# Kernel tuning notes

Hardware: AMD Instinct MI355X
Metric: run time of the kernel (lower is better)

## Reference

```python
import jax, jax.numpy as jnp
import numpy as np

NEG = -1.0e9


def setup_inputs() -> dict:
    key = jax.random.key(0)
    ks = jax.random.split(key, 8)
    B, L, D = 4, 2048, 1024
    s = 1.0 / np.sqrt(D)
    return {
        "x": jax.random.normal(ks[0], (B, L, D), dtype=jnp.float32),
        "Wq": jax.random.normal(ks[1], (D, D), dtype=jnp.float32) * s,
        "bq": jax.random.normal(ks[2], (D,), dtype=jnp.float32) * 0.02,
        "Wk": jax.random.normal(ks[3], (D, D), dtype=jnp.float32) * s,
        "bk": jax.random.normal(ks[4], (D,), dtype=jnp.float32) * 0.02,
        "Wv": jax.random.normal(ks[5], (D, D), dtype=jnp.float32) * s,
        "bv": jax.random.normal(ks[6], (D,), dtype=jnp.float32) * 0.02,
        "lengths": jax.random.randint(ks[7], (B,), 1, 2048, dtype=jnp.int32),
    }


def reference(x, Wq, bq, Wk, bk, Wv, bv, lengths):
    # x: [B, L, D]; single-head self-attention with causal + length additive masks
    B, L, D = x.shape
    q = x @ Wq + bq  # [B, L, D]
    k = x @ Wk + bk
    v = x @ Wv + bv
    scale = 1.0 / jnp.sqrt(jnp.asarray(D, dtype=x.dtype))
    att = jnp.einsum("bid,bjd->bij", q, k) * scale  # [B, L, L]
    idx = jnp.arange(L)
    causal = jnp.where(idx[None, :] > idx[:, None], NEG, 0.0).astype(x.dtype)  # [L, L]
    # length mask: NEG where j >= len[b] or i >= len[b]
    invalid = (idx[None, :] >= lengths[:, None])  # [B, L]
    lenmask = jnp.where(invalid[:, :, None] | invalid[:, None, :], NEG, 0.0).astype(x.dtype)
    att = att + causal[None, :, :] + lenmask
    att = jax.nn.softmax(att, axis=-1)
    return jnp.einsum("bij,bjd->bid", att, v)
```

## Files before the change

### kernel.cpp

```cpp
#include <hip/hip_runtime.h>

#define NEGV (-1.0e9f)

typedef __bf16 bf16_t;
typedef __bf16 bf16x8 __attribute__((ext_vector_type(8)));
typedef __bf16 bf16x4 __attribute__((ext_vector_type(4)));
typedef float  f32x4  __attribute__((ext_vector_type(4)));

__device__ __forceinline__ void gld16(const void* g, void* l) {
    __builtin_amdgcn_global_load_lds(
        (const __attribute__((address_space(1))) void*)g,
        (__attribute__((address_space(3))) void*)l, 16, 0, 0);
}


#define STG(P0, P1, BASE, NB, HOFS) do {               \
    gld16(P0, (BASE) + (NB) * 32768 + (HOFS));         \
    gld16(P1, (BASE) + (NB) * 32768 + (HOFS) + 8192);  \
    P0 += 64; P1 += 64; } while (0)

#define MMROW(ai)                                                                                    \
    acc[ib + ai][0] = __builtin_amdgcn_mfma_f32_16x16x32_bf16(a##ai, b0, acc[ib + ai][0], 0, 0, 0);  \
    acc[ib + ai][1] = __builtin_amdgcn_mfma_f32_16x16x32_bf16(a##ai, b1, acc[ib + ai][1], 0, 0, 0);  \
    acc[ib + ai][2] = __builtin_amdgcn_mfma_f32_16x16x32_bf16(a##ai, b2, acc[ib + ai][2], 0, 0, 0);  \
    acc[ib + ai][3] = __builtin_amdgcn_mfma_f32_16x16x32_bf16(a##ai, b3, acc[ib + ai][3], 0, 0, 0)

#define PHASE(BUFO, HOFS, PK, STAGE_STMT, ENDW) do {                     \
    bf16x8 a0 = *(const bf16x8*)(rdA + (BUFO) + (HOFS)        + (PK));   \
    bf16x8 a1 = *(const bf16x8*)(rdA + (BUFO) + (HOFS) + 2048 + (PK));   \
    bf16x8 a2 = *(const bf16x8*)(rdA + (BUFO) + (HOFS) + 4096 + (PK));   \
    bf16x8 a3 = *(const bf16x8*)(rdA + (BUFO) + (HOFS) + 6144 + (PK));   \
    bf16x8 b0 = *(const bf16x8*)(rdB + (BUFO)          + (PK));          \
    bf16x8 b1 = *(const bf16x8*)(rdB + (BUFO) + 2048   + (PK));          \
    bf16x8 b2 = *(const bf16x8*)(rdB + (BUFO) + 4096   + (PK));          \
    bf16x8 b3 = *(const bf16x8*)(rdB + (BUFO) + 6144   + (PK));          \
    STAGE_STMT;                                                          \
    __builtin_amdgcn_s_barrier();                                        \
    asm volatile("s_waitcnt lgkmcnt(0)" ::: "memory");                   \
    __builtin_amdgcn_s_setprio(1);                                       \
    {                                                                    \
        const int ib = (HOFS) ? 4 : 0;                                   \
        MMROW(0); MMROW(1); MMROW(2); MMROW(3);                          \
    }                                                                    \
    __builtin_amdgcn_s_setprio(0);                                       \
    ENDW;                                                                \
    __builtin_amdgcn_s_barrier();                                        \
} while (0)

__device__ __forceinline__ void mainloop256(
    const bf16_t* __restrict__ A, const bf16_t* __restrict__ B,
    int ldA, int ldB, int nkt, char* smem, int tid, f32x4 acc[8][4])
{
    const int w    = tid >> 6;
    const int lane = tid & 63;
    const int wm   = w & 1;
    const int wn   = w >> 1;
    const int l16  = lane & 15;
    const int quad = lane >> 4;

    const int r0 = tid >> 3;
    const int c0 = ((tid & 7) ^ (r0 & 7)) * 8;
    const int s1 = 512 + tid;
    const int r1 = s1 >> 3;
    const int c1 = ((s1 & 7) ^ (r1 & 7)) * 8;

    const bf16_t* pa00 = A + (size_t)(r0)       * ldA + c0;
    const bf16_t* pa01 = A + (size_t)(r1)       * ldA + c1;
    const bf16_t* pa10 = A + (size_t)(128 + r0) * ldA + c0;
    const bf16_t* pa11 = A + (size_t)(128 + r1) * ldA + c1;
    const bf16_t* pb00 = B + (size_t)(r0)       * ldB + c0;
    const bf16_t* pb01 = B + (size_t)(r1)       * ldB + c1;
    const bf16_t* pb10 = B + (size_t)(128 + r0) * ldB + c0;
    const bf16_t* pb11 = B + (size_t)(128 + r1) * ldB + c1;

    char* const stA = smem + (w << 10);
    char* const stB = smem + 65536 + (w << 10);

    const int pk0 = ((quad    ) ^ (l16 & 7)) << 4;
    const int pk1 = ((quad + 4) ^ (l16 & 7)) << 4;
    const char* rdA = smem +         ((wm << 7) + l16) * 128;
    const char* rdB = smem + 65536 + ((wn << 6) + l16) * 128;

    STG(pa00, pa01, stA, 0, 0);
    STG(pa10, pa11, stA, 0, 16384);
    STG(pb00, pb01, stB, 0, 0);
    STG(pb10, pb11, stB, 0, 16384);
    asm volatile("s_waitcnt vmcnt(0)" ::: "memory");
    __builtin_amdgcn_s_barrier();

    for (int kt = 0; kt < nkt; ++kt) {
        const int bufo = (kt & 1) << 15;
        const int nb   = (kt & 1) ^ 1;
        const bool st  = (kt + 1) < nkt;
        PHASE(bufo, 0,    pk0, if (st) STG(pa00, pa01, stA, nb, 0),     );
        PHASE(bufo, 0,    pk1, if (st) STG(pa10, pa11, stA, nb, 16384), );
        PHASE(bufo, 8192, pk0, if (st) STG(pb00, pb01, stB, nb, 0),     );
        PHASE(bufo, 8192, pk1, if (st) STG(pb10, pb11, stB, nb, 16384),
              asm volatile("s_waitcnt vmcnt(0)" ::: "memory"));
    }
}

__global__ __launch_bounds__(256)
void convert_x_kernel(const float* __restrict__ x, bf16_t* __restrict__ xb)
{
    const size_t i = ((size_t)blockIdx.x * 256 + threadIdx.x) * 8;
    float4 a = *(const float4*)&x[i];
    float4 b = *(const float4*)&x[i + 4];
    bf16x8 o;
    o[0] = (bf16_t)a.x; o[1] = (bf16_t)a.y; o[2] = (bf16_t)a.z; o[3] = (bf16_t)a.w;
    o[4] = (bf16_t)b.x; o[5] = (bf16_t)b.y; o[6] = (bf16_t)b.z; o[7] = (bf16_t)b.w;
    *(bf16x8*)&xb[i] = o;
}

__global__ __launch_bounds__(256)
void transpose_w_kernel(const float* __restrict__ W0, const float* __restrict__ W1,
                        const float* __restrict__ W2, bf16_t* __restrict__ WT)
{
    __shared__ float t[32][33];
    const float* W = (blockIdx.z == 0) ? W0 : (blockIdx.z == 1) ? W1 : W2;
    bf16_t* WTz = WT + (size_t)blockIdx.z * 1024 * 1024;
    const int k0 = blockIdx.y * 32, n0 = blockIdx.x * 32;
    const int r = threadIdx.x >> 3, c4 = (threadIdx.x & 7) * 4;
    float4 v = *(const float4*)&W[(size_t)(k0 + r) * 1024 + n0 + c4];
    t[r][c4 + 0] = v.x; t[r][c4 + 1] = v.y; t[r][c4 + 2] = v.z; t[r][c4 + 3] = v.w;
    __syncthreads();
    bf16x4 o;
#pragma unroll
    for (int j = 0; j < 4; ++j) o[j] = (bf16_t)t[c4 + j][r];
    *(bf16x4*)&WTz[(size_t)(n0 + r) * 1024 + k0 + c4] = o;
}

__global__ __launch_bounds__(512, 2)
void gemm_qk256(const bf16_t* __restrict__ A, const bf16_t* __restrict__ Bt,
                const float* __restrict__ bq, const float* __restrict__ bk,
                bf16_t* __restrict__ C, int N, int Kd)
{
    __shared__ __align__(16) char smem[131072];
    int bid = blockIdx.y * 8 + blockIdx.x;
    bid = (bid & 7) * 32 + (bid >> 3);
    const int n0 = (bid & 7) * 256;
    const int m0 = (bid >> 3) * 256;
    const int tid = threadIdx.x;

    f32x4 acc[8][4];
#pragma unroll
    for (int i = 0; i < 8; ++i)
#pragma unroll
        for (int j = 0; j < 4; ++j) acc[i][j] = (f32x4)(0.0f);

    mainloop256(A + (size_t)m0 * Kd, Bt + (size_t)n0 * Kd, Kd, Kd, Kd >> 6,
                smem, tid, acc);

    const int w = tid >> 6, lane = tid & 63;
    const int wm = w & 1, wn = w >> 1, quad = lane >> 4, l16 = lane & 15;
#pragma unroll
    for (int j = 0; j < 4; ++j) {
        const int col = n0 + wn * 64 + j * 16 + l16;
        const float bval = (col < 1024) ? bq[col] : bk[col - 1024];
#pragma unroll
        for (int i = 0; i < 8; ++i) {
            const int row = m0 + wm * 128 + i * 16 + quad * 4;
#pragma unroll
            for (int r = 0; r < 4; ++r)
                C[(size_t)(row + r) * N + col] = (bf16_t)(acc[i][j][r] + bval);
        }
    }
}

__global__ __launch_bounds__(512, 2)
void gemm_vt256(const bf16_t* __restrict__ WvT, const bf16_t* __restrict__ xb,
                const float* __restrict__ bv, bf16_t* __restrict__ VT,
                int N, int Kd)
{
    __shared__ __align__(16) char smem[131072];
    const int m0 = blockIdx.y * 256, n0 = blockIdx.x * 256;
    const int tid = threadIdx.x;

    f32x4 acc[8][4];
#pragma unroll
    for (int i = 0; i < 8; ++i)
#pragma unroll
        for (int j = 0; j < 4; ++j) acc[i][j] = (f32x4)(0.0f);

    mainloop256(WvT + (size_t)m0 * Kd, xb + (size_t)n0 * Kd, Kd, Kd, Kd >> 6,
                smem, tid, acc);

    const int w = tid >> 6, lane = tid & 63;
    const int wm = w & 1, wn = w >> 1, quad = lane >> 4, l16 = lane & 15;
#pragma unroll
    for (int i = 0; i < 8; ++i) {
        const int row = m0 + wm * 128 + i * 16 + quad * 4;
#pragma unroll
        for (int r = 0; r < 4; ++r) {
            const float bval = bv[row + r];
#pragma unroll
            for (int j = 0; j < 4; ++j) {
                const int col = n0 + wn * 64 + j * 16 + l16;
                VT[(size_t)(row + r) * N + col] = (bf16_t)(acc[i][j][r] + bval);
            }
        }
    }
}

__global__ __launch_bounds__(512, 2)
void scores256(const bf16_t* __restrict__ Q, const bf16_t* __restrict__ K,
               int ldq, const int* __restrict__ lengths,
               float* __restrict__ S, int L, int Dd, float alpha)
{
    __shared__ __align__(16) char smem[131072];
    const int b = blockIdx.z;
    const int len = lengths[b];
    int it = 0;
    while ((it + 1) * (it + 2) / 2 <= (int)blockIdx.x) ++it;
    const int jt = blockIdx.x - it * (it + 1) / 2;
    const int m0 = it * 256, n0 = jt * 256;
    float* Sb = S + (size_t)b * L * L;
    const int tid = threadIdx.x;

    f32x4 acc[8][4];
#pragma unroll
    for (int i = 0; i < 8; ++i)
#pragma unroll
        for (int j = 0; j < 4; ++j) acc[i][j] = (f32x4)(0.0f);

    const bf16_t* Qb = Q + (size_t)b * L * ldq + (size_t)m0 * ldq;
    const bf16_t* Kb = K + (size_t)b * L * ldq + (size_t)n0 * ldq;
    mainloop256(Qb, Kb, ldq, ldq, Dd >> 6, smem, tid, acc);

    const int w = tid >> 6, lane = tid & 63;
    const int wm = w & 1, wn = w >> 1, quad = lane >> 4, l16 = lane & 15;
#pragma unroll
    for (int i = 0; i < 8; ++i) {
#pragma unroll
        for (int j = 0; j < 4; ++j) {
            const int col = n0 + wn * 64 + j * 16 + l16;
#pragma unroll
            for (int r = 0; r < 4; ++r) {
                const int row = m0 + wm * 128 + i * 16 + quad * 4 + r;
                float s = acc[i][j][r] * alpha;
                if (col > row) s += NEGV;
                if (row >= len || col >= len) s += NEGV;
                Sb[(size_t)row * L + col] = s;
            }
        }
    }
}

__global__ __launch_bounds__(256)
void softmax_kernel(const float* __restrict__ S, bf16_t* __restrict__ P,
                    int L, int ldp)
{
    __shared__ float red[8];
    const int i = blockIdx.x;
    const int bound  = ((i >> 7) + 1) << 7;
    const int bound2 = ((i >> 8) + 1) << 8;
    const float* row = S + ((size_t)blockIdx.y * L + i) * L;
    bf16_t* prow = P + ((size_t)blockIdx.y * L + i) * ldp;
    const int t = threadIdx.x;
    const int w = t >> 6, lane = t & 63;
    const int j8 = t * 8;
    const bool act = j8 < bound;

    float v[8];
    float m = -3.0e38f;
    if (act) {
        float4 a = *(const float4*)&row[j8];
        float4 b = *(const float4*)&row[j8 + 4];
        v[0] = a.x; v[1] = a.y; v[2] = a.z; v[3] = a.w;
        v[4] = b.x; v[5] = b.y; v[6] = b.z; v[7] = b.w;
#pragma unroll
        for (int j = 0; j < 8; ++j) m = fmaxf(m, v[j]);
    }
#pragma unroll
    for (int off = 32; off > 0; off >>= 1) m = fmaxf(m, __shfl_down(m, off, 64));
    if (lane == 0) red[w] = m;
    __syncthreads();
    m = fmaxf(fmaxf(red[0], red[1]), fmaxf(red[2], red[3]));

    float s = 0.f;
    if (act) {
#pragma unroll
        for (int j = 0; j < 8; ++j) {
            v[j] = __expf(v[j] - m);
            s += v[j];
        }
    }
#pragma unroll
    for (int off = 32; off > 0; off >>= 1) s += __shfl_down(s, off, 64);
    if (lane == 0) red[4 + w] = s;
    __syncthreads();
    s = red[4] + red[5] + red[6] + red[7];

    if (act) {
        const float inv = 1.0f / s;
        bf16x8 o;
#pragma unroll
        for (int j = 0; j < 8; ++j) o[j] = (bf16_t)(v[j] * inv);
        *(bf16x8*)&prow[j8] = o;
    } else if (j8 < bound2) {
        bf16x8 z;
#pragma unroll
        for (int j = 0; j < 8; ++j) z[j] = (bf16_t)0.0f;
        *(bf16x8*)&prow[j8] = z;
    }
}

__global__ __launch_bounds__(512, 2)
void pv256(const bf16_t* __restrict__ P, int ldp,
           const bf16_t* __restrict__ VT, int ldv,
           float* __restrict__ O, int L, int Dd)
{
    __shared__ __align__(16) char smem[131072];
    const int b = blockIdx.z;
    const int mt = gridDim.y - 1 - blockIdx.y;
    const int m0 = mt * 256, n0 = blockIdx.x * 256;
    const int tid = threadIdx.x;

    f32x4 acc[8][4];
#pragma unroll
    for (int i = 0; i < 8; ++i)
#pragma unroll
        for (int j = 0; j < 4; ++j) acc[i][j] = (f32x4)(0.0f);

    const int nkt = (m0 + 256) >> 6;
    const bf16_t* Pb = P + (size_t)b * L * ldp + (size_t)m0 * ldp;
    const bf16_t* Vb = VT + (size_t)b * L + (size_t)n0 * ldv;
    mainloop256(Pb, Vb, ldp, ldv, nkt, smem, tid, acc);

    float* Ob = O + (size_t)b * L * Dd;
    const int w = tid >> 6, lane = tid & 63;
    const int wm = w & 1, wn = w >> 1, quad = lane >> 4, l16 = lane & 15;
#pragma unroll
    for (int i = 0; i < 8; ++i) {
        const int row = m0 + wm * 128 + i * 16 + quad * 4;
#pragma unroll
        for (int j = 0; j < 4; ++j) {
            const int col = n0 + wn * 64 + j * 16 + l16;
#pragma unroll
            for (int r = 0; r < 4; ++r)
                Ob[(size_t)(row + r) * Dd + col] = acc[i][j][r];
        }
    }
}

extern "C" void kernel_launch(void* const* d_in, const int* in_sizes, int n_in,
                              void* d_out, int out_size, void* d_ws, size_t ws_size,
                              hipStream_t stream)
{
    const float* x  = (const float*)d_in[0];
    const float* Wq = (const float*)d_in[1];
    const float* bq = (const float*)d_in[2];
    const float* Wk = (const float*)d_in[3];
    const float* bk = (const float*)d_in[4];
    const float* Wv = (const float*)d_in[5];
    const float* bv = (const float*)d_in[6];
    const int*  len = (const int*)d_in[7];
    float* out = (float*)d_out;

    const int B = 4, L = 2048, D = 1024;
    const int M = B * L;
    const int N2 = 2 * D;

    bf16_t* xb = (bf16_t*)d_ws;
    bf16_t* WT = xb + (size_t)M * D;
    bf16_t* QK = WT + (size_t)3 * D * D;
    bf16_t* VT = QK + (size_t)M * N2;
    float*  S  = (float*)(VT + (size_t)D * M);
    bf16_t* P  = QK;

    convert_x_kernel<<<(M * D) / 2048, 256, 0, stream>>>(x, xb);

    transpose_w_kernel<<<dim3(32, 32, 3), 256, 0, stream>>>(Wq, Wk, Wv, WT);

    gemm_qk256<<<dim3(8, 32), 512, 0, stream>>>(xb, WT, bq, bk, QK, N2, D);

    gemm_vt256<<<dim3(32, 4), 512, 0, stream>>>(
        WT + (size_t)2 * D * D, xb, bv, VT, M, D);

    scores256<<<dim3(36, 1, B), 512, 0, stream>>>(
        QK, QK + 1024, N2, len, S, L, D, 0.03125f);

    softmax_kernel<<<dim3(L, B), 256, 0, stream>>>(S, P, L, N2);

    pv256<<<dim3(4, 8, 4), 512, 0, stream>>>(P, N2, VT, M, out, L, D);
}
```

Measured before the change: 280.7 us.

## Use 256x128 GEMM tiles for V projection, scores and PV kernels

Adds a new 256x128 tiled mainloop with its own LDS staging and MFMA phase structure, and switches the V projection, causal scores and PV GEMMs to it with doubled grid sizes. The intent is to fill more of the GPU's compute units, since the earlier 256x256 grids (128, 144 and 128 blocks) underfilled the device. Smaller tiles lower arithmetic intensity and raise global and LDS traffic per FLOP. The scores kernel's triangular block indexing is rewritten for two column tiles per row tile.

```diff
diff --git a/kernel.cpp b/kernel.cpp
--- a/kernel.cpp
+++ b/kernel.cpp
@@ -100,6 +100,88 @@
     }
 }
 
+
+#define STG2(P0, P1, DST) do {                                   \
+    gld16(P0, (DST)); gld16(P1, (char*)(DST) + 8192);            \
+    P0 += 64; P1 += 64; } while (0)
+
+#define MM2ROW(ai)                                                                         \
+    acc[ai][0] = __builtin_amdgcn_mfma_f32_16x16x32_bf16(a##ai, b0, acc[ai][0], 0, 0, 0);  \
+    acc[ai][1] = __builtin_amdgcn_mfma_f32_16x16x32_bf16(a##ai, b1, acc[ai][1], 0, 0, 0);  \
+    acc[ai][2] = __builtin_amdgcn_mfma_f32_16x16x32_bf16(a##ai, b2, acc[ai][2], 0, 0, 0);  \
+    acc[ai][3] = __builtin_amdgcn_mfma_f32_16x16x32_bf16(a##ai, b3, acc[ai][3], 0, 0, 0)
+
+#define PHASEX(AOFS, BOFS, PK, STAGE_STMT, ENDW) do {                  \
+    bf16x8 a0 = *(const bf16x8*)(rdA + (AOFS)        + (PK));          \
+    bf16x8 a1 = *(const bf16x8*)(rdA + (AOFS) + 2048 + (PK));          \
+    bf16x8 a2 = *(const bf16x8*)(rdA + (AOFS) + 4096 + (PK));          \
+    bf16x8 a3 = *(const bf16x8*)(rdA + (AOFS) + 6144 + (PK));          \
+    bf16x8 b0 = *(const bf16x8*)(rdB + (BOFS)        + (PK));          \
+    bf16x8 b1 = *(const bf16x8*)(rdB + (BOFS) + 2048 + (PK));          \
+    bf16x8 b2 = *(const bf16x8*)(rdB + (BOFS) + 4096 + (PK));          \
+    bf16x8 b3 = *(const bf16x8*)(rdB + (BOFS) + 6144 + (PK));          \
+    STAGE_STMT;                                                        \
+    __builtin_amdgcn_s_barrier();                                      \
+    asm volatile("s_waitcnt lgkmcnt(0)" ::: "memory");                 \
+    __builtin_amdgcn_s_setprio(1);                                     \
+    MM2ROW(0); MM2ROW(1); MM2ROW(2); MM2ROW(3);                        \
+    __builtin_amdgcn_s_setprio(0);                                     \
+    ENDW;                                                              \
+    __builtin_amdgcn_s_barrier();                                      \
+} while (0)
+
+__device__ __forceinline__ void mainloop256x128(
+    const bf16_t* __restrict__ A, const bf16_t* __restrict__ B,
+    int ldA, int ldB, int nkt, char* smem, int tid, f32x4 acc[4][4])
+{
+    const int w    = tid >> 6;
+    const int lane = tid & 63;
+    const int wm   = w & 3;
+    const int wn   = w >> 2;
+    const int l16  = lane & 15;
+    const int quad = lane >> 4;
+
+    const int r0 = tid >> 3;
+    const int c0 = ((tid & 7) ^ (r0 & 7)) * 8;
+    const int s1 = 512 + tid;
+    const int r1 = s1 >> 3;
+    const int c1 = ((s1 & 7) ^ (r1 & 7)) * 8;
+
+    const bf16_t* pa00 = A + (size_t)(r0)       * ldA + c0;
+    const bf16_t* pa01 = A + (size_t)(r1)       * ldA + c1;
+    const bf16_t* pa10 = A + (size_t)(128 + r0) * ldA + c0;
+    const bf16_t* pa11 = A + (size_t)(128 + r1) * ldA + c1;
+    const bf16_t* pb0  = B + (size_t)(r0)       * ldB + c0;
+    const bf16_t* pb1  = B + (size_t)(r1)       * ldB + c1;
+
+    char* const stA = smem + (w << 10);
+    char* const stB = smem + 65536 + (w << 10);
+
+    const int pk0 = ((quad    ) ^ (l16 & 7)) << 4;
+    const int pk1 = ((quad + 4) ^ (l16 & 7)) << 4;
+    const char* rdA = smem +         ((wm << 6) + l16) * 128;
+    const char* rdB = smem + 65536 + ((wn << 6) + l16) * 128;
+
+    STG2(pa00, pa01, stA);
+    STG2(pa10, pa11, stA + 16384);
+    STG2(pb0,  pb1,  stB);
+    asm volatile("s_waitcnt vmcnt(0)" ::: "memory");
+    __builtin_amdgcn_s_barrier();
+
+    for (int kt = 0; kt < nkt; ++kt) {
+        const int aofs = (kt & 1) << 15;
+        const int bofs = (kt & 1) << 14;
+        char* const nA = stA + ((((kt & 1) ^ 1)) << 15);
+        char* const nB = stB + ((((kt & 1) ^ 1)) << 14);
+        const bool st  = (kt + 1) < nkt;
+        PHASEX(aofs, bofs, pk0,
+               if (st) { STG2(pa00, pa01, nA); STG2(pa10, pa11, nA + 16384); }, );
+        PHASEX(aofs, bofs, pk1,
+               if (st) { STG2(pb0, pb1, nB); },
+               asm volatile("s_waitcnt vmcnt(0)" ::: "memory"));
+    }
+}
+
 __global__ __launch_bounds__(256)
 void convert_x_kernel(const float* __restrict__ x, bf16_t* __restrict__ xb)
 {
@@ -172,24 +254,25 @@
                 const float* __restrict__ bv, bf16_t* __restrict__ VT,
                 int N, int Kd)
 {
-    __shared__ __align__(16) char smem[131072];
-    const int m0 = blockIdx.y * 256, n0 = blockIdx.x * 256;
+    __shared__ __align__(16) char smem[98304];
+    const int m0 = blockIdx.y * 256;
+    const int n0 = blockIdx.x * 128;
     const int tid = threadIdx.x;
 
-    f32x4 acc[8][4];
-#pragma unroll
-    for (int i = 0; i < 8; ++i)
+    f32x4 acc[4][4];
+#pragma unroll
+    for (int i = 0; i < 4; ++i)
 #pragma unroll
         for (int j = 0; j < 4; ++j) acc[i][j] = (f32x4)(0.0f);
 
-    mainloop256(WvT + (size_t)m0 * Kd, xb + (size_t)n0 * Kd, Kd, Kd, Kd >> 6,
-                smem, tid, acc);
+    mainloop256x128(WvT + (size_t)m0 * Kd, xb + (size_t)n0 * Kd, Kd, Kd, Kd >> 6,
+                    smem, tid, acc);
 
     const int w = tid >> 6, lane = tid & 63;
-    const int wm = w & 1, wn = w >> 1, quad = lane >> 4, l16 = lane & 15;
-#pragma unroll
-    for (int i = 0; i < 8; ++i) {
-        const int row = m0 + wm * 128 + i * 16 + quad * 4;
+    const int wm = w & 3, wn = w >> 2, quad = lane >> 4, l16 = lane & 15;
+#pragma unroll
+    for (int i = 0; i < 4; ++i) {
+        const int row = m0 + wm * 64 + i * 16 + quad * 4;
 #pragma unroll
         for (int r = 0; r < 4; ++r) {
             const float bval = bv[row + r];
@@ -207,36 +290,36 @@
                int ldq, const int* __restrict__ lengths,
                float* __restrict__ S, int L, int Dd, float alpha)
 {
-    __shared__ __align__(16) char smem[131072];
+    __shared__ __align__(16) char smem[98304];
     const int b = blockIdx.z;
     const int len = lengths[b];
-    int it = 0;
-    while ((it + 1) * (it + 2) / 2 <= (int)blockIdx.x) ++it;
-    const int jt = blockIdx.x - it * (it + 1) / 2;
-    const int m0 = it * 256, n0 = jt * 256;
+    int mt = 0;
+    while ((mt + 1) * (mt + 2) <= (int)blockIdx.x) ++mt;
+    const int jt = blockIdx.x - mt * (mt + 1);
+    const int m0 = mt * 256, n0 = jt * 128;
     float* Sb = S + (size_t)b * L * L;
     const int tid = threadIdx.x;
 
-    f32x4 acc[8][4];
-#pragma unroll
-    for (int i = 0; i < 8; ++i)
+    f32x4 acc[4][4];
+#pragma unroll
+    for (int i = 0; i < 4; ++i)
 #pragma unroll
         for (int j = 0; j < 4; ++j) acc[i][j] = (f32x4)(0.0f);
 
     const bf16_t* Qb = Q + (size_t)b * L * ldq + (size_t)m0 * ldq;
     const bf16_t* Kb = K + (size_t)b * L * ldq + (size_t)n0 * ldq;
-    mainloop256(Qb, Kb, ldq, ldq, Dd >> 6, smem, tid, acc);
+    mainloop256x128(Qb, Kb, ldq, ldq, Dd >> 6, smem, tid, acc);
 
     const int w = tid >> 6, lane = tid & 63;
-    const int wm = w & 1, wn = w >> 1, quad = lane >> 4, l16 = lane & 15;
-#pragma unroll
-    for (int i = 0; i < 8; ++i) {
+    const int wm = w & 3, wn = w >> 2, quad = lane >> 4, l16 = lane & 15;
+#pragma unroll
+    for (int i = 0; i < 4; ++i) {
 #pragma unroll
         for (int j = 0; j < 4; ++j) {
             const int col = n0 + wn * 64 + j * 16 + l16;
 #pragma unroll
             for (int r = 0; r < 4; ++r) {
-                const int row = m0 + wm * 128 + i * 16 + quad * 4 + r;
+                const int row = m0 + wm * 64 + i * 16 + quad * 4 + r;
                 float s = acc[i][j][r] * alpha;
                 if (col > row) s += NEGV;
                 if (row >= len || col >= len) s += NEGV;
@@ -310,29 +393,29 @@
            const bf16_t* __restrict__ VT, int ldv,
            float* __restrict__ O, int L, int Dd)
 {
-    __shared__ __align__(16) char smem[131072];
+    __shared__ __align__(16) char smem[98304];
     const int b = blockIdx.z;
     const int mt = gridDim.y - 1 - blockIdx.y;
-    const int m0 = mt * 256, n0 = blockIdx.x * 256;
+    const int m0 = mt * 256, n0 = blockIdx.x * 128;
     const int tid = threadIdx.x;
 
-    f32x4 acc[8][4];
-#pragma unroll
-    for (int i = 0; i < 8; ++i)
+    f32x4 acc[4][4];
+#pragma unroll
+    for (int i = 0; i < 4; ++i)
 #pragma unroll
         for (int j = 0; j < 4; ++j) acc[i][j] = (f32x4)(0.0f);
 
     const int nkt = (m0 + 256) >> 6;
     const bf16_t* Pb = P + (size_t)b * L * ldp + (size_t)m0 * ldp;
     const bf16_t* Vb = VT + (size_t)b * L + (size_t)n0 * ldv;
-    mainloop256(Pb, Vb, ldp, ldv, nkt, smem, tid, acc);
+    mainloop256x128(Pb, Vb, ldp, ldv, nkt, smem, tid, acc);
 
     float* Ob = O + (size_t)b * L * Dd;
     const int w = tid >> 6, lane = tid & 63;
-    const int wm = w & 1, wn = w >> 1, quad = lane >> 4, l16 = lane & 15;
-#pragma unroll
-    for (int i = 0; i < 8; ++i) {
-        const int row = m0 + wm * 128 + i * 16 + quad * 4;
+    const int wm = w & 3, wn = w >> 2, quad = lane >> 4, l16 = lane & 15;
+#pragma unroll
+    for (int i = 0; i < 4; ++i) {
+        const int row = m0 + wm * 64 + i * 16 + quad * 4;
 #pragma unroll
         for (int j = 0; j < 4; ++j) {
             const int col = n0 + wn * 64 + j * 16 + l16;
@@ -374,13 +457,13 @@
 
     gemm_qk256<<<dim3(8, 32), 512, 0, stream>>>(xb, WT, bq, bk, QK, N2, D);
 
-    gemm_vt256<<<dim3(32, 4), 512, 0, stream>>>(
+    gemm_vt256<<<dim3(64, 4), 512, 0, stream>>>(
         WT + (size_t)2 * D * D, xb, bv, VT, M, D);
 
-    scores256<<<dim3(36, 1, B), 512, 0, stream>>>(
+    scores256<<<dim3(72, 1, B), 512, 0, stream>>>(
         QK, QK + 1024, N2, len, S, L, D, 0.03125f);
 
     softmax_kernel<<<dim3(L, B), 256, 0, stream>>>(S, P, L, N2);
 
-    pv256<<<dim3(4, 8, 4), 512, 0, stream>>>(P, N2, VT, M, out, L, D);
-}
+    pv256<<<dim3(8, 8, 4), 512, 0, stream>>>(P, N2, VT, M, out, L, D);
+}
```

After: 259.9 us. -7.4%, faster.

## Rework GEMM mainloop to triple-buffered BK=32 and 256x128 tiles for V/PV

Applied to the files above, without the earlier changes.

Replaces the shared double-buffered 64-wide-K mainloop with a triple-buffered 32-wide-K pipeline that prefetches two stages ahead and needs one barrier per iteration instead of several. It splits LDS fragment waits so the first half of the MFMAs can start before all reads land. It also adds a 256x128 tile variant for the V projection and PV kernels, which doubles their grids and adds block-index swizzling. The goal is to hide global-to-LDS latency, cut barrier stalls and improve load balance, at the cost of more loop iterations and a new LDS swizzle layout that must stay conflict-free.

```diff
diff --git a/kernel.cpp b/kernel.cpp
--- a/kernel.cpp
+++ b/kernel.cpp
@@ -14,90 +14,142 @@
 }
 
 
-#define STG(P0, P1, BASE, NB, HOFS) do {               \
-    gld16(P0, (BASE) + (NB) * 32768 + (HOFS));         \
-    gld16(P1, (BASE) + (NB) * 32768 + (HOFS) + 8192);  \
-    P0 += 64; P1 += 64; } while (0)
-
-#define MMROW(ai)                                                                                    \
-    acc[ib + ai][0] = __builtin_amdgcn_mfma_f32_16x16x32_bf16(a##ai, b0, acc[ib + ai][0], 0, 0, 0);  \
-    acc[ib + ai][1] = __builtin_amdgcn_mfma_f32_16x16x32_bf16(a##ai, b1, acc[ib + ai][1], 0, 0, 0);  \
-    acc[ib + ai][2] = __builtin_amdgcn_mfma_f32_16x16x32_bf16(a##ai, b2, acc[ib + ai][2], 0, 0, 0);  \
-    acc[ib + ai][3] = __builtin_amdgcn_mfma_f32_16x16x32_bf16(a##ai, b3, acc[ib + ai][3], 0, 0, 0)
-
-#define PHASE(BUFO, HOFS, PK, STAGE_STMT, ENDW) do {                     \
-    bf16x8 a0 = *(const bf16x8*)(rdA + (BUFO) + (HOFS)        + (PK));   \
-    bf16x8 a1 = *(const bf16x8*)(rdA + (BUFO) + (HOFS) + 2048 + (PK));   \
-    bf16x8 a2 = *(const bf16x8*)(rdA + (BUFO) + (HOFS) + 4096 + (PK));   \
-    bf16x8 a3 = *(const bf16x8*)(rdA + (BUFO) + (HOFS) + 6144 + (PK));   \
-    bf16x8 b0 = *(const bf16x8*)(rdB + (BUFO)          + (PK));          \
-    bf16x8 b1 = *(const bf16x8*)(rdB + (BUFO) + 2048   + (PK));          \
-    bf16x8 b2 = *(const bf16x8*)(rdB + (BUFO) + 4096   + (PK));          \
-    bf16x8 b3 = *(const bf16x8*)(rdB + (BUFO) + 6144   + (PK));          \
-    STAGE_STMT;                                                          \
-    __builtin_amdgcn_s_barrier();                                        \
-    asm volatile("s_waitcnt lgkmcnt(0)" ::: "memory");                   \
-    __builtin_amdgcn_s_setprio(1);                                       \
-    {                                                                    \
-        const int ib = (HOFS) ? 4 : 0;                                   \
-        MMROW(0); MMROW(1); MMROW(2); MMROW(3);                          \
-    }                                                                    \
-    __builtin_amdgcn_s_setprio(0);                                       \
-    ENDW;                                                                \
-    __builtin_amdgcn_s_barrier();                                        \
-} while (0)
-
-__device__ __forceinline__ void mainloop256(
+#define MMR(AF, IB)                                                                        \
+    acc[IB][0] = __builtin_amdgcn_mfma_f32_16x16x32_bf16(AF, b0, acc[IB][0], 0, 0, 0);     \
+    acc[IB][1] = __builtin_amdgcn_mfma_f32_16x16x32_bf16(AF, b1, acc[IB][1], 0, 0, 0);     \
+    acc[IB][2] = __builtin_amdgcn_mfma_f32_16x16x32_bf16(AF, b2, acc[IB][2], 0, 0, 0);     \
+    acc[IB][3] = __builtin_amdgcn_mfma_f32_16x16x32_bf16(AF, b3, acc[IB][3], 0, 0, 0)
+
+__device__ __forceinline__ void ml256x256(
     const bf16_t* __restrict__ A, const bf16_t* __restrict__ B,
     int ldA, int ldB, int nkt, char* smem, int tid, f32x4 acc[8][4])
 {
-    const int w    = tid >> 6;
-    const int lane = tid & 63;
-    const int wm   = w & 1;
-    const int wn   = w >> 1;
-    const int l16  = lane & 15;
-    const int quad = lane >> 4;
-
-    const int r0 = tid >> 3;
-    const int c0 = ((tid & 7) ^ (r0 & 7)) * 8;
-    const int s1 = 512 + tid;
-    const int r1 = s1 >> 3;
-    const int c1 = ((s1 & 7) ^ (r1 & 7)) * 8;
-
-    const bf16_t* pa00 = A + (size_t)(r0)       * ldA + c0;
-    const bf16_t* pa01 = A + (size_t)(r1)       * ldA + c1;
-    const bf16_t* pa10 = A + (size_t)(128 + r0) * ldA + c0;
-    const bf16_t* pa11 = A + (size_t)(128 + r1) * ldA + c1;
-    const bf16_t* pb00 = B + (size_t)(r0)       * ldB + c0;
-    const bf16_t* pb01 = B + (size_t)(r1)       * ldB + c1;
-    const bf16_t* pb10 = B + (size_t)(128 + r0) * ldB + c0;
-    const bf16_t* pb11 = B + (size_t)(128 + r1) * ldB + c1;
-
+    const int w = tid >> 6, lane = tid & 63;
+    const int wm = w & 1, wn = w >> 1;
+    const int l16 = lane & 15, quad = lane >> 4;
+
+    const int g0 = 2 * (tid >> 3) + ((tid >> 2) & 1);
+    const int c0 = ((tid & 3) ^ ((tid >> 3) & 3)) * 8;
+    const bf16_t* pa0 = A + (size_t)g0 * ldA + c0;
+    const bf16_t* pa1 = pa0 + (size_t)128 * ldA;
+    const bf16_t* pb0 = B + (size_t)g0 * ldB + c0;
+    const bf16_t* pb1 = pb0 + (size_t)128 * ldB;
     char* const stA = smem + (w << 10);
-    char* const stB = smem + 65536 + (w << 10);
-
-    const int pk0 = ((quad    ) ^ (l16 & 7)) << 4;
-    const int pk1 = ((quad + 4) ^ (l16 & 7)) << 4;
-    const char* rdA = smem +         ((wm << 7) + l16) * 128;
-    const char* rdB = smem + 65536 + ((wn << 6) + l16) * 128;
-
-    STG(pa00, pa01, stA, 0, 0);
-    STG(pa10, pa11, stA, 0, 16384);
-    STG(pb00, pb01, stB, 0, 0);
-    STG(pb10, pb11, stB, 0, 16384);
-    asm volatile("s_waitcnt vmcnt(0)" ::: "memory");
+    char* const stB = smem + 16384 + (w << 10);
+
+    const int rowo = (l16 >> 1) * 128 + (l16 & 1) * 64 + ((quad ^ ((l16 >> 1) & 3)) << 4);
+    const char* rdA = smem + (wm << 13) + rowo;
+    const char* rdB = smem + 16384 + (wn << 12) + rowo;
+
+#define STG6(BO) do { gld16(pa0, stA + (BO)); gld16(pa1, stA + (BO) + 8192);   \
+                      gld16(pb0, stB + (BO)); gld16(pb1, stB + (BO) + 8192);   \
+                      pa0 += 32; pa1 += 32; pb0 += 32; pb1 += 32; } while (0)
+
+    STG6(0);
+    if (nkt > 1) {
+        STG6(32768);
+        asm volatile("s_waitcnt vmcnt(4)" ::: "memory");
+    } else {
+        asm volatile("s_waitcnt vmcnt(0)" ::: "memory");
+    }
     __builtin_amdgcn_s_barrier();
 
+    int ro = 0, so = 65536;
     for (int kt = 0; kt < nkt; ++kt) {
-        const int bufo = (kt & 1) << 15;
-        const int nb   = (kt & 1) ^ 1;
-        const bool st  = (kt + 1) < nkt;
-        PHASE(bufo, 0,    pk0, if (st) STG(pa00, pa01, stA, nb, 0),     );
-        PHASE(bufo, 0,    pk1, if (st) STG(pa10, pa11, stA, nb, 16384), );
-        PHASE(bufo, 8192, pk0, if (st) STG(pb00, pb01, stB, nb, 0),     );
-        PHASE(bufo, 8192, pk1, if (st) STG(pb10, pb11, stB, nb, 16384),
-              asm volatile("s_waitcnt vmcnt(0)" ::: "memory"));
-    }
+        const char* ra = rdA + ro;
+        const char* rb = rdB + ro;
+        bf16x8 a0 = *(const bf16x8*)(ra);
+        bf16x8 a1 = *(const bf16x8*)(ra + 1024);
+        bf16x8 a2 = *(const bf16x8*)(ra + 2048);
+        bf16x8 a3 = *(const bf16x8*)(ra + 3072);
+        bf16x8 b0 = *(const bf16x8*)(rb);
+        bf16x8 b1 = *(const bf16x8*)(rb + 1024);
+        bf16x8 b2 = *(const bf16x8*)(rb + 2048);
+        bf16x8 b3 = *(const bf16x8*)(rb + 3072);
+        bf16x8 a4 = *(const bf16x8*)(ra + 4096);
+        bf16x8 a5 = *(const bf16x8*)(ra + 5120);
+        bf16x8 a6 = *(const bf16x8*)(ra + 6144);
+        bf16x8 a7 = *(const bf16x8*)(ra + 7168);
+        const bool st = (kt + 2) < nkt;
+        if (st) STG6(so);
+        asm volatile("s_waitcnt lgkmcnt(4)" ::: "memory");
+        __builtin_amdgcn_sched_barrier(0);
+        __builtin_amdgcn_s_setprio(1);
+        MMR(a0, 0); MMR(a1, 1); MMR(a2, 2); MMR(a3, 3);
+        __builtin_amdgcn_s_setprio(0);
+        asm volatile("s_waitcnt lgkmcnt(0)" ::: "memory");
+        __builtin_amdgcn_sched_barrier(0);
+        __builtin_amdgcn_s_setprio(1);
+        MMR(a4, 4); MMR(a5, 5); MMR(a6, 6); MMR(a7, 7);
+        __builtin_amdgcn_s_setprio(0);
+        if (st) asm volatile("s_waitcnt vmcnt(4)" ::: "memory");
+        else    asm volatile("s_waitcnt vmcnt(0)" ::: "memory");
+        __builtin_amdgcn_s_barrier();
+        ro = (ro == 65536) ? 0 : (ro + 32768);
+        so = (so == 65536) ? 0 : (so + 32768);
+    }
+#undef STG6
+}
+
+__device__ __forceinline__ void ml256x128(
+    const bf16_t* __restrict__ A, const bf16_t* __restrict__ B,
+    int ldA, int ldB, int nkt, char* smem, int tid, f32x4 acc[4][4])
+{
+    const int w = tid >> 6, lane = tid & 63;
+    const int wm = w & 3, wn = w >> 2;
+    const int l16 = lane & 15, quad = lane >> 4;
+
+    const int g0 = 2 * (tid >> 3) + ((tid >> 2) & 1);
+    const int c0 = ((tid & 3) ^ ((tid >> 3) & 3)) * 8;
+    const bf16_t* pa0 = A + (size_t)g0 * ldA + c0;
+    const bf16_t* pa1 = pa0 + (size_t)128 * ldA;
+    const bf16_t* pb0 = B + (size_t)g0 * ldB + c0;
+    char* const stA = smem + (w << 10);
+    char* const stB = smem + 16384 + (w << 10);
+
+    const int rowo = (l16 >> 1) * 128 + (l16 & 1) * 64 + ((quad ^ ((l16 >> 1) & 3)) << 4);
+    const char* rdA = smem + (wm << 12) + rowo;
+    const char* rdB = smem + 16384 + (wn << 12) + rowo;
+
+#define STG3(BO) do { gld16(pa0, stA + (BO)); gld16(pa1, stA + (BO) + 8192);   \
+                      gld16(pb0, stB + (BO));                                  \
+                      pa0 += 32; pa1 += 32; pb0 += 32; } while (0)
+
+    STG3(0);
+    if (nkt > 1) {
+        STG3(24576);
+        asm volatile("s_waitcnt vmcnt(3)" ::: "memory");
+    } else {
+        asm volatile("s_waitcnt vmcnt(0)" ::: "memory");
+    }
+    __builtin_amdgcn_s_barrier();
+
+    int ro = 0, so = 49152;
+    for (int kt = 0; kt < nkt; ++kt) {
+        const char* ra = rdA + ro;
+        const char* rb = rdB + ro;
+        bf16x8 a0 = *(const bf16x8*)(ra);
+        bf16x8 a1 = *(const bf16x8*)(ra + 1024);
+        bf16x8 a2 = *(const bf16x8*)(ra + 2048);
+        bf16x8 a3 = *(const bf16x8*)(ra + 3072);
+        bf16x8 b0 = *(const bf16x8*)(rb);
+        bf16x8 b1 = *(const bf16x8*)(rb + 1024);
+        bf16x8 b2 = *(const bf16x8*)(rb + 2048);
+        bf16x8 b3 = *(const bf16x8*)(rb + 3072);
+        const bool st = (kt + 2) < nkt;
+        if (st) STG3(so);
+        asm volatile("s_waitcnt lgkmcnt(0)" ::: "memory");
+        __builtin_amdgcn_sched_barrier(0);
+        __builtin_amdgcn_s_setprio(1);
+        MMR(a0, 0); MMR(a1, 1); MMR(a2, 2); MMR(a3, 3);
+        __builtin_amdgcn_s_setprio(0);
+        if (st) asm volatile("s_waitcnt vmcnt(3)" ::: "memory");
+        else    asm volatile("s_waitcnt vmcnt(0)" ::: "memory");
+        __builtin_amdgcn_s_barrier();
+        ro = (ro == 49152) ? 0 : (ro + 24576);
+        so = (so == 49152) ? 0 : (so + 24576);
+    }
+#undef STG3
 }
 
 __global__ __launch_bounds__(256)
@@ -135,7 +187,7 @@
                 const float* __restrict__ bq, const float* __restrict__ bk,
                 bf16_t* __restrict__ C, int N, int Kd)
 {
-    __shared__ __align__(16) char smem[131072];
+    __shared__ __align__(16) char smem[98304];
     int bid = blockIdx.y * 8 + blockIdx.x;
     bid = (bid & 7) * 32 + (bid >> 3);
     const int n0 = (bid & 7) * 256;
@@ -148,8 +200,8 @@
 #pragma unroll
         for (int j = 0; j < 4; ++j) acc[i][j] = (f32x4)(0.0f);
 
-    mainloop256(A + (size_t)m0 * Kd, Bt + (size_t)n0 * Kd, Kd, Kd, Kd >> 6,
-                smem, tid, acc);
+    ml256x256(A + (size_t)m0 * Kd, Bt + (size_t)n0 * Kd, Kd, Kd, Kd >> 5,
+              smem, tid, acc);
 
     const int w = tid >> 6, lane = tid & 63;
     const int wm = w & 1, wn = w >> 1, quad = lane >> 4, l16 = lane & 15;
@@ -172,24 +224,27 @@
                 const float* __restrict__ bv, bf16_t* __restrict__ VT,
                 int N, int Kd)
 {
-    __shared__ __align__(16) char smem[131072];
-    const int m0 = blockIdx.y * 256, n0 = blockIdx.x * 256;
+    __shared__ __align__(16) char smem[73728];
+    int bid = blockIdx.y * 64 + blockIdx.x;
+    bid = (bid & 7) * 32 + (bid >> 3);
+    const int m0 = (bid >> 6) * 256;
+    const int n0 = (bid & 63) * 128;
     const int tid = threadIdx.x;
 
-    f32x4 acc[8][4];
-#pragma unroll
-    for (int i = 0; i < 8; ++i)
+    f32x4 acc[4][4];
+#pragma unroll
+    for (int i = 0; i < 4; ++i)
 #pragma unroll
         for (int j = 0; j < 4; ++j) acc[i][j] = (f32x4)(0.0f);
 
-    mainloop256(WvT + (size_t)m0 * Kd, xb + (size_t)n0 * Kd, Kd, Kd, Kd >> 6,
-                smem, tid, acc);
-
-    const int w = tid >> 6, lane = tid & 63;
-    const int wm = w & 1, wn = w >> 1, quad = lane >> 4, l16 = lane & 15;
-#pragma unroll
-    for (int i = 0; i < 8; ++i) {
-        const int row = m0 + wm * 128 + i * 16 + quad * 4;
+    ml256x128(WvT + (size_t)m0 * Kd, xb + (size_t)n0 * Kd, Kd, Kd, Kd >> 5,
+              smem, tid, acc);
+
+    const int w = tid >> 6, lane = tid & 63;
+    const int wm = w & 3, wn = w >> 2, quad = lane >> 4, l16 = lane & 15;
+#pragma unroll
+    for (int i = 0; i < 4; ++i) {
+        const int row = m0 + wm * 64 + i * 16 + quad * 4;
 #pragma unroll
         for (int r = 0; r < 4; ++r) {
             const float bval = bv[row + r];
@@ -207,7 +262,7 @@
                int ldq, const int* __restrict__ lengths,
                float* __restrict__ S, int L, int Dd, float alpha)
 {
-    __shared__ __align__(16) char smem[131072];
+    __shared__ __align__(16) char smem[98304];
     const int b = blockIdx.z;
     const int len = lengths[b];
     int it = 0;
@@ -225,7 +280,7 @@
 
     const bf16_t* Qb = Q + (size_t)b * L * ldq + (size_t)m0 * ldq;
     const bf16_t* Kb = K + (size_t)b * L * ldq + (size_t)n0 * ldq;
-    mainloop256(Qb, Kb, ldq, ldq, Dd >> 6, smem, tid, acc);
+    ml256x256(Qb, Kb, ldq, ldq, Dd >> 5, smem, tid, acc);
 
     const int w = tid >> 6, lane = tid & 63;
     const int wm = w & 1, wn = w >> 1, quad = lane >> 4, l16 = lane & 15;
@@ -310,29 +365,31 @@
            const bf16_t* __restrict__ VT, int ldv,
            float* __restrict__ O, int L, int Dd)
 {
-    __shared__ __align__(16) char smem[131072];
+    __shared__ __align__(16) char smem[73728];
     const int b = blockIdx.z;
-    const int mt = gridDim.y - 1 - blockIdx.y;
-    const int m0 = mt * 256, n0 = blockIdx.x * 256;
+    int bid = blockIdx.y * 8 + blockIdx.x;
+    bid = (bid & 7) * 8 + (bid >> 3);
+    const int mt = 7 - (bid >> 3);
+    const int m0 = mt * 256, n0 = (bid & 7) * 128;
     const int tid = threadIdx.x;
 
-    f32x4 acc[8][4];
-#pragma unroll
-    for (int i = 0; i < 8; ++i)
+    f32x4 acc[4][4];
+#pragma unroll
+    for (int i = 0; i < 4; ++i)
 #pragma unroll
         for (int j = 0; j < 4; ++j) acc[i][j] = (f32x4)(0.0f);
 
-    const int nkt = (m0 + 256) >> 6;
+    const int nkt = (m0 + 256) >> 5;
     const bf16_t* Pb = P + (size_t)b * L * ldp + (size_t)m0 * ldp;
     const bf16_t* Vb = VT + (size_t)b * L + (size_t)n0 * ldv;
-    mainloop256(Pb, Vb, ldp, ldv, nkt, smem, tid, acc);
+    ml256x128(Pb, Vb, ldp, ldv, nkt, smem, tid, acc);
 
     float* Ob = O + (size_t)b * L * Dd;
     const int w = tid >> 6, lane = tid & 63;
-    const int wm = w & 1, wn = w >> 1, quad = lane >> 4, l16 = lane & 15;
-#pragma unroll
-    for (int i = 0; i < 8; ++i) {
-        const int row = m0 + wm * 128 + i * 16 + quad * 4;
+    const int wm = w & 3, wn = w >> 2, quad = lane >> 4, l16 = lane & 15;
+#pragma unroll
+    for (int i = 0; i < 4; ++i) {
+        const int row = m0 + wm * 64 + i * 16 + quad * 4;
 #pragma unroll
         for (int j = 0; j < 4; ++j) {
             const int col = n0 + wn * 64 + j * 16 + l16;
@@ -374,7 +431,7 @@
 
     gemm_qk256<<<dim3(8, 32), 512, 0, stream>>>(xb, WT, bq, bk, QK, N2, D);
 
-    gemm_vt256<<<dim3(32, 4), 512, 0, stream>>>(
+    gemm_vt256<<<dim3(64, 4), 512, 0, stream>>>(
         WT + (size_t)2 * D * D, xb, bv, VT, M, D);
 
     scores256<<<dim3(36, 1, B), 512, 0, stream>>>(
@@ -382,5 +439,5 @@
 
     softmax_kernel<<<dim3(L, B), 256, 0, stream>>>(S, P, L, N2);
 
-    pv256<<<dim3(4, 8, 4), 512, 0, stream>>>(P, N2, VT, M, out, L, D);
-}
+    pv256<<<dim3(8, 8, 4), 512, 0, stream>>>(P, N2, VT, M, out, L, D);
+}
```

New measurement: 244.0 us. -13.1%, faster.
